# Kernel optimization log

Measured on AMD Instinct MI355X. Metric: run time of the kernel, lower is better.

The kernel has to match this reference:

```python
import jax, jax.numpy as jnp
import numpy as np

K = 20
EPS = 1e-5  # BatchNorm eps, eval mode with running_mean=0, running_var=1


def _bn(x, g, b):
    # eval-mode BatchNorm with running stats (mean=0, var=1): affine only
    return x * (g / jnp.sqrt(1.0 + EPS)) + b


def _lrelu(x):
    return jax.nn.leaky_relu(x, 0.2)


def setup_inputs() -> dict:
    key = jax.random.key(0)
    ks = jax.random.split(key, 8)
    B, N, EMB, OUT = 8, 4096, 1024, 128
    def w(k, shape):
        fan_in = shape[0]
        return (jax.random.normal(k, shape, jnp.float32) / np.sqrt(fan_in)).astype(jnp.float32)
    inp = {
        "x":  jax.random.normal(ks[0], (B, N, 3), jnp.float32),
        "W1": w(ks[1], (6, 64)),   "g1": jnp.ones(64),  "b1": jnp.zeros(64),
        "W2": w(ks[2], (64, 64)),  "g2": jnp.ones(64),  "b2": jnp.zeros(64),
        "W3": w(ks[3], (64, 128)), "g3": jnp.ones(128), "b3": jnp.zeros(128),
        "W4": w(ks[4], (128, 256)),"g4": jnp.ones(256), "b4": jnp.zeros(256),
        "W5": w(ks[5], (512, EMB)),"g5": jnp.ones(EMB), "b5": jnp.zeros(EMB),
        "L1": w(ks[6], (2 * EMB, 512)), "g6": jnp.ones(512), "b6": jnp.zeros(512),
        "L2": w(ks[7], (512, 256)), "L2b": jnp.zeros(256), "g7": jnp.ones(256), "b7": jnp.zeros(256),
        "L3": w(jax.random.fold_in(key, 99), (256, OUT)), "L3b": jnp.zeros(OUT),
    }
    return inp


def _knn_idx(pts):
    # pts: [B, 3, N]; returns indices of K nearest neighbors [B, N, K]
    inner = -2.0 * jnp.einsum('bdn,bdm->bnm', pts, pts)  # [B,N,N]
    xx = jnp.sum(pts * pts, axis=1)                       # [B,N]
    pd = -xx[:, :, None] - inner - xx[:, None, :]          # negative squared distance
    return jax.lax.top_k(pd, K)[1]                         # [B,N,K]


def reference(x, W1, g1, b1, W2, g2, b2, W3, g3, b3, W4, g4, b4,
              W5, g5, b5, L1, g6, b6, L2, L2b, g7, b7, L3, L3b):
    B, N, _ = x.shape
    pts = jnp.transpose(x, (0, 2, 1))           # [B,3,N]
    idx = _knn_idx(pts)                          # [B,N,K]

    # gather neighbor coordinates: [B,N,K,3]
    feature = jax.vmap(lambda xb, ib: xb[ib])(x, idx)
    center = jnp.broadcast_to(x[:, :, None, :], (B, N, K, 3))
    h = jnp.concatenate([feature, center], axis=-1)  # [B,N,K,6]

    h = _lrelu(_bn(jnp.einsum('bnkc,co->bnko', h, W1), g1, b1))
    x1 = jnp.max(h, axis=2)                          # [B,N,64]
    h = _lrelu(_bn(jnp.einsum('bnkc,co->bnko', h, W2), g2, b2))
    x2 = jnp.max(h, axis=2)                          # [B,N,64]
    h = _lrelu(_bn(jnp.einsum('bnkc,co->bnko', h, W3), g3, b3))
    x3 = jnp.max(h, axis=2)                          # [B,N,128]
    h = _lrelu(_bn(jnp.einsum('bnkc,co->bnko', h, W4), g4, b4))
    x4 = jnp.max(h, axis=2)                          # [B,N,256]

    hc = jnp.concatenate([x1, x2, x3, x4], axis=-1)  # [B,N,512]
    h5 = _lrelu(_bn(jnp.einsum('bnc,co->bno', hc, W5), g5, b5))  # [B,N,EMB]

    gmax = jnp.max(h5, axis=1)                       # [B,EMB]
    gavg = jnp.mean(h5, axis=1)                      # [B,EMB]
    g = jnp.concatenate([gmax, gavg], axis=-1)       # [B,2*EMB]

    f = _lrelu(_bn(g @ L1, g6, b6))                  # dropout = identity (eval)
    f = _lrelu(_bn(f @ L2 + L2b, g7, b7))
    return f @ L3 + L3b                              # [B,OUT]
```

## Files before the change

### kernel.cpp

```cpp
#include <hip/hip_runtime.h>
#include <hip/hip_bf16.h>
#include <hip/hip_fp16.h>

#define NPTS 4096
#define KNB  20
#define EPSB 1e-5f

typedef _Float16 half8  __attribute__((ext_vector_type(8)));
typedef _Float16 half2v __attribute__((ext_vector_type(2)));
typedef float    f32x4  __attribute__((ext_vector_type(4)));

__device__ __forceinline__ f32x4 mfma16(half8 a, half8 b, f32x4 c){
  return __builtin_amdgcn_mfma_f32_16x16x32_f16(a, b, c, 0, 0, 0);
}

__device__ __forceinline__ half8 loadA_lds(const _Float16* buf, int C, int mt, int ks, int lane){
  int row = mt*16 + (lane & 15);
  int k0  = ks*32 + (lane >> 4)*8;
  int e   = (row*C + k0) ^ ((row & 7) << 3);
  return *reinterpret_cast<const half8*>(&buf[e]);
}

__device__ __forceinline__ half8 loadB_g(const _Float16* WT, int K, int nt, int ks, int lane){
  int col = nt*16 + (lane & 15);
  int k0  = ks*32 + (lane >> 4)*8;
  return *reinterpret_cast<const half8*>(&WT[col*K + k0]);
}

__device__ __forceinline__ half2v pkmax(half2v a, half2v b){
  return __builtin_elementwise_max(a, b);
}
__device__ __forceinline__ half2v shflx_h2(half2v v, int m){
  int iv = __builtin_bit_cast(int, v);
  iv = __shfl_xor(iv, m);
  return __builtin_bit_cast(half2v, iv);
}
__device__ __forceinline__ half2v ep_pk(float a, float b, half2v sc2, half2v bs2){
  half2v v = __builtin_bit_cast(half2v, __builtin_amdgcn_cvt_pkrtz(a, b));
  v = v*sc2 + bs2;
  half2v w = v * (half2v){(_Float16)0.2f, (_Float16)0.2f};
  return pkmax(v, w);
}

__global__ __launch_bounds__(1024)
void knn_kernel(const float* __restrict__ x, int* __restrict__ idx_out){
  __shared__ float4 spts[NPTS];
  int b  = blockIdx.x >> 8;
  int r0 = (blockIdx.x & 255) << 4;
  const float* xb = x + (size_t)b*NPTS*3;
  for (int t = threadIdx.x; t < NPTS; t += 1024){
    float px = xb[t*3+0], py = xb[t*3+1], pz = xb[t*3+2];
    spts[t] = make_float4(px, py, pz, 0.5f*(px*px + py*py + pz*pz));
  }
  __syncthreads();
  int wave = threadIdx.x >> 6, lane = threadIdx.x & 63;
  int i = r0 + wave;
  float4 pi = spts[i];
  float b1 = -INFINITY, b2 = -INFINITY, b3 = -INFINITY;
  int   i1 = 0, i2 = 0, i3 = 0;
  #pragma unroll 8
  for (int t = 0; t < 64; ++t){
    int j = (t << 6) + lane;
    float4 q = spts[j];
    float d = pi.x*q.x + pi.y*q.y + pi.z*q.z - pi.w - q.w;
    bool c1 = d > b1, c2 = d > b2, c3 = d > b3;
    float t2 = fmaxf(b2, fminf(b1, d));
    float t3 = fmaxf(b3, fminf(b2, d));
    i3 = c2 ? i2 : (c3 ? j : i3);
    i2 = c1 ? i1 : (c2 ? j : i2);
    i1 = c1 ? j : i1;
    b1 = fmaxf(b1, d);
    b2 = t2; b3 = t3;
  }
  unsigned long long rem = 0ull;
  size_t obase = ((size_t)b*NPTS + i)*KNB;
  #pragma unroll 1
  for (int kk = 0; kk < KNB; ++kk){
    unsigned s = __float_as_uint(b1);
    unsigned key = s ^ ((unsigned)(((int)s) >> 31) | 0x80000000u);
    key = (key & 0xFFFFFFC0u) | (unsigned)lane;
    unsigned bv = key;
    #pragma unroll
    for (int m = 1; m <= 32; m <<= 1){
      unsigned ov = (unsigned)__shfl_xor((int)bv, m);
      bv = bv > ov ? bv : ov;
    }
    int wl = (int)(bv & 63u);
    int bj = __shfl(i1, wl);
    if (lane == 0) idx_out[obase + kk] = bj;
    bool iw = (lane == wl);
    unsigned long long nbit = 1ull << (i1 >> 6);
    rem |= iw ? nbit : 0ull;
    b1 = iw ? b2 : b1;  i1 = iw ? i2 : i1;
    b2 = iw ? b3 : b2;  i2 = iw ? i3 : i2;
    b3 = iw ? -INFINITY : b3;
    if (kk < KNB-1 && __any(b1 == -INFINITY)){
      if (b1 == -INFINITY){
        b2 = -INFINITY; b3 = -INFINITY; i1 = 0; i2 = 0; i3 = 0;
        #pragma unroll 8
        for (int t = 0; t < 64; ++t){
          if (rem & (1ull << t)) continue;
          int j = (t << 6) + lane;
          float4 q = spts[j];
          float d = pi.x*q.x + pi.y*q.y + pi.z*q.z - pi.w - q.w;
          bool c1 = d > b1, c2 = d > b2, c3 = d > b3;
          float t2 = fmaxf(b2, fminf(b1, d));
          float t3 = fmaxf(b3, fminf(b2, d));
          i3 = c2 ? i2 : (c3 ? j : i3);
          i2 = c1 ? i1 : (c2 ? j : i2);
          i1 = c1 ? j : i1;
          b1 = fmaxf(b1, d);
          b2 = t2; b3 = t3;
        }
      }
    }
  }
}

__global__ __launch_bounds__(256)
void prep_kernel(const float* __restrict__ W2, const float* __restrict__ W3,
                 const float* __restrict__ W4,
                 _Float16* __restrict__ W2T, _Float16* __restrict__ W3T,
                 _Float16* __restrict__ W4T){
  int t = blockIdx.x*256 + threadIdx.x;
  if (t < 4096){ int o=t>>6, k=t&63;                W2T[t] = (_Float16)W2[k*64+o]; }
  else if (t < 12288){ int u=t-4096;  int o=u>>6, k=u&63;   W3T[u] = (_Float16)W3[k*128+o]; }
  else if (t < 45056){ int u=t-12288; int o=u>>7, k=u&127;  W4T[u] = (_Float16)W4[k*256+o]; }
}

__global__ __launch_bounds__(256)
void prep5_kernel(const float* __restrict__ W5, _Float16* __restrict__ W5T){
  __shared__ float tile[32][33];
  int tk = (blockIdx.x & 15) << 5;
  int to = (blockIdx.x >> 4) << 5;
  int lr = threadIdx.x >> 5;
  int lc = threadIdx.x & 31;
  #pragma unroll
  for (int r = 0; r < 32; r += 8)
    tile[lr + r][lc] = W5[(size_t)(tk + lr + r)*1024 + to + lc];
  __syncthreads();
  #pragma unroll
  for (int r = 0; r < 32; r += 8)
    W5T[(size_t)(to + lr + r)*512 + tk + lc] = (_Float16)tile[lc][lr + r];
}

__device__ __forceinline__ void pk_bucket(int mt, bool c1, bool c2, bool c3, half2v m,
                                          half2v& q0, half2v& q1, half2v& q2, half2v& q3){
  const half2v NI = {(_Float16)-INFINITY, (_Float16)-INFINITY};
  if (mt == 0)      q0 = pkmax(q0, m);
  else if (mt == 4) q3 = pkmax(q3, m);
  else if (mt == 1){ q1 = pkmax(q1, c1 ? m : NI); q0 = pkmax(q0, c1 ? NI : m); }
  else if (mt == 2){ q2 = pkmax(q2, c2 ? m : NI); q1 = pkmax(q1, c2 ? NI : m); }
  else             { q3 = pkmax(q3, c3 ? m : NI); q2 = pkmax(q2, c3 ? NI : m); }
}

__device__ __forceinline__ void reduce_write_pk(half2v q0, half2v q1, half2v q2, half2v q3,
                                                _Float16* __restrict__ hc, size_t gp0,
                                                int off, int g, int c){
  q0 = pkmax(q0, shflx_h2(q0,16)); q0 = pkmax(q0, shflx_h2(q0,32));
  q1 = pkmax(q1, shflx_h2(q1,16)); q1 = pkmax(q1, shflx_h2(q1,32));
  q2 = pkmax(q2, shflx_h2(q2,16)); q2 = pkmax(q2, shflx_h2(q2,32));
  q3 = pkmax(q3, shflx_h2(q3,16)); q3 = pkmax(q3, shflx_h2(q3,32));
  half2v v = (g == 0) ? q0 : (g == 1) ? q1 : (g == 2) ? q2 : q3;
  _Float16 r = v.x > v.y ? v.x : v.y;
  hc[(gp0 + g)*512 + off + c] = r;
}

__global__ __launch_bounds__(256)
void edge_kernel(const float* __restrict__ x, const int* __restrict__ knn,
                 const float* __restrict__ W1, const float* __restrict__ g1, const float* __restrict__ b1,
                 const _Float16* __restrict__ W2T, const float* __restrict__ g2, const float* __restrict__ b2,
                 const _Float16* __restrict__ W3T, const float* __restrict__ g3, const float* __restrict__ b3,
                 const _Float16* __restrict__ W4T, const float* __restrict__ g4, const float* __restrict__ b4,
                 _Float16* __restrict__ hc){
  __shared__ __align__(16) char smem[40960];
  _Float16* hb1 = (_Float16*)(smem);
  _Float16* hb2 = (_Float16*)(smem + 10240);
  _Float16* hb3 = (_Float16*)(smem + 20480);
  float*    h0f = (float*)(smem + 20480);
  float*    h0c = (float*)(smem + 20480 + 1280);
  const float rs = 1.f / sqrtf(1.f + EPSB);
  const half2v NI = {(_Float16)-INFINITY, (_Float16)-INFINITY};
  int gp0 = blockIdx.x << 2;
  int b   = gp0 >> 12;
  int n0  = gp0 & (NPTS-1);
  const float* xb = x + (size_t)b*NPTS*3;
  int tid = threadIdx.x;
  if (tid < 80){
    int p = tid / 20, k = tid % 20;
    int nb = knn[((size_t)b*NPTS + n0 + p)*KNB + k];
    h0f[tid*4+0] = xb[nb*3+0];
    h0f[tid*4+1] = xb[nb*3+1];
    h0f[tid*4+2] = xb[nb*3+2];
  } else if (tid < 96){
    int u = tid - 80; int p = u >> 2, c = u & 3;
    if (c < 3) h0c[p*4+c] = xb[(n0+p)*3+c];
  }
  __syncthreads();
  int w = tid >> 6, lane = tid & 63, g = lane >> 4, cc = lane & 15;
  bool c1 = (g >= 1), c2 = (g >= 2), c3 = (g >= 3);
  {
    int col = lane;
    float sc = g1[col]*rs, bs = b1[col];
    float w0=W1[col], w1_=W1[64+col], w2_=W1[128+col], w3_=W1[192+col], w4_=W1[256+col], w5_=W1[320+col];
    float cx = h0c[w*4+0], cy = h0c[w*4+1], cz = h0c[w*4+2];
    float m1 = -INFINITY;
    #pragma unroll 5
    for (int k = 0; k < KNB; ++k){
      int r = w*20 + k;
      float a = h0f[r*4+0]*w0 + h0f[r*4+1]*w1_ + h0f[r*4+2]*w2_ + cx*w3_ + cy*w4_ + cz*w5_;
      float vv = a*sc + bs; vv = vv > 0.f ? vv : 0.2f*vv;
      hb1[((r<<6)+col) ^ ((r&7)<<3)] = (_Float16)vv;
      m1 = fmaxf(m1, vv);
    }
    hc[(size_t)(gp0 + w)*512 + col] = (_Float16)m1;
  }
  __syncthreads();
  {
    int colg = (w<<4) + cc;
    float scf = g2[colg]*rs, bsf = b2[colg];
    half2v sc2 = {(_Float16)scf,(_Float16)scf}, bs2 = {(_Float16)bsf,(_Float16)bsf};
    half8 bf0 = loadB_g(W2T, 64, w, 0, lane);
    half8 bf1 = loadB_g(W2T, 64, w, 1, lane);
    half2v q0=NI, q1=NI, q2=NI, q3=NI;
    #pragma unroll
    for (int mt = 0; mt < 5; ++mt){
      f32x4 a = {0.f,0.f,0.f,0.f};
      a = mfma16(loadA_lds(hb1,64,mt,0,lane), bf0, a);
      a = mfma16(loadA_lds(hb1,64,mt,1,lane), bf1, a);
      half2v lo = ep_pk(a[0], a[1], sc2, bs2);
      half2v hi = ep_pk(a[2], a[3], sc2, bs2);
      int r0_ = mt*16 + g*4;
      hb2[((r0_+0)*64+colg) ^ (((r0_+0)&7)<<3)] = lo.x;
      hb2[((r0_+1)*64+colg) ^ (((r0_+1)&7)<<3)] = lo.y;
      hb2[((r0_+2)*64+colg) ^ (((r0_+2)&7)<<3)] = hi.x;
      hb2[((r0_+3)*64+colg) ^ (((r0_+3)&7)<<3)] = hi.y;
      pk_bucket(mt, c1, c2, c3, pkmax(lo,hi), q0, q1, q2, q3);
    }
    reduce_write_pk(q0,q1,q2,q3, hc, gp0, 64 + (w<<4), g, cc);
  }
  __syncthreads();
  {
    int ntA = (w<<1), ntB = ntA + 1;
    int colA = (ntA<<4) + cc, colB = (ntB<<4) + cc;
    float sAf = g3[colA]*rs, bAf = b3[colA];
    float sBf = g3[colB]*rs, bBf = b3[colB];
    half2v scA2={(_Float16)sAf,(_Float16)sAf}, bsA2={(_Float16)bAf,(_Float16)bAf};
    half2v scB2={(_Float16)sBf,(_Float16)sBf}, bsB2={(_Float16)bBf,(_Float16)bBf};
    half8 bA0 = loadB_g(W3T, 64, ntA, 0, lane);
    half8 bA1 = loadB_g(W3T, 64, ntA, 1, lane);
    half8 bB0 = loadB_g(W3T, 64, ntB, 0, lane);
    half8 bB1 = loadB_g(W3T, 64, ntB, 1, lane);
    half2v qA0=NI,qA1=NI,qA2=NI,qA3=NI, qB0=NI,qB1=NI,qB2=NI,qB3=NI;
    #pragma unroll
    for (int mt = 0; mt < 5; ++mt){
      half8 a0 = loadA_lds(hb2,64,mt,0,lane);
      half8 a1 = loadA_lds(hb2,64,mt,1,lane);
      f32x4 aA = {0.f,0.f,0.f,0.f};
      aA = mfma16(a0, bA0, aA); aA = mfma16(a1, bA1, aA);
      f32x4 aB = {0.f,0.f,0.f,0.f};
      aB = mfma16(a0, bB0, aB); aB = mfma16(a1, bB1, aB);
      half2v loA = ep_pk(aA[0],aA[1],scA2,bsA2);
      half2v hiA = ep_pk(aA[2],aA[3],scA2,bsA2);
      half2v loB = ep_pk(aB[0],aB[1],scB2,bsB2);
      half2v hiB = ep_pk(aB[2],aB[3],scB2,bsB2);
      int r0_ = mt*16 + g*4;
      hb3[((r0_+0)*128+colA) ^ (((r0_+0)&7)<<3)] = loA.x;
      hb3[((r0_+1)*128+colA) ^ (((r0_+1)&7)<<3)] = loA.y;
      hb3[((r0_+2)*128+colA) ^ (((r0_+2)&7)<<3)] = hiA.x;
      hb3[((r0_+3)*128+colA) ^ (((r0_+3)&7)<<3)] = hiA.y;
      hb3[((r0_+0)*128+colB) ^ (((r0_+0)&7)<<3)] = loB.x;
      hb3[((r0_+1)*128+colB) ^ (((r0_+1)&7)<<3)] = loB.y;
      hb3[((r0_+2)*128+colB) ^ (((r0_+2)&7)<<3)] = hiB.x;
      hb3[((r0_+3)*128+colB) ^ (((r0_+3)&7)<<3)] = hiB.y;
      pk_bucket(mt, c1, c2, c3, pkmax(loA,hiA), qA0,qA1,qA2,qA3);
      pk_bucket(mt, c1, c2, c3, pkmax(loB,hiB), qB0,qB1,qB2,qB3);
    }
    reduce_write_pk(qA0,qA1,qA2,qA3, hc, gp0, 128 + (ntA<<4), g, cc);
    reduce_write_pk(qB0,qB1,qB2,qB3, hc, gp0, 128 + (ntB<<4), g, cc);
  }
  __syncthreads();
  #pragma unroll 1
  for (int pass = 0; pass < 2; ++pass){
    int ntA = (pass<<3) + w, ntB = ntA + 4;
    int colA = (ntA<<4) + cc, colB = (ntB<<4) + cc;
    float sAf = g4[colA]*rs, bAf = b4[colA];
    float sBf = g4[colB]*rs, bBf = b4[colB];
    half2v scA2={(_Float16)sAf,(_Float16)sAf}, bsA2={(_Float16)bAf,(_Float16)bAf};
    half2v scB2={(_Float16)sBf,(_Float16)sBf}, bsB2={(_Float16)bBf,(_Float16)bBf};
    half8 bwA[4], bwB[4];
    #pragma unroll
    for (int ks = 0; ks < 4; ++ks){
      bwA[ks] = loadB_g(W4T, 128, ntA, ks, lane);
      bwB[ks] = loadB_g(W4T, 128, ntB, ks, lane);
    }
    half2v qA0=NI,qA1=NI,qA2=NI,qA3=NI, qB0=NI,qB1=NI,qB2=NI,qB3=NI;
    #pragma unroll
    for (int mt = 0; mt < 5; ++mt){
      half8 a[4];
      #pragma unroll
      for (int ks = 0; ks < 4; ++ks) a[ks] = loadA_lds(hb3,128,mt,ks,lane);
      f32x4 aA = {0.f,0.f,0.f,0.f};
      #pragma unroll
      for (int ks = 0; ks < 4; ++ks) aA = mfma16(a[ks], bwA[ks], aA);
      f32x4 aB = {0.f,0.f,0.f,0.f};
      #pragma unroll
      for (int ks = 0; ks < 4; ++ks) aB = mfma16(a[ks], bwB[ks], aB);
      half2v mA = pkmax(ep_pk(aA[0],aA[1],scA2,bsA2), ep_pk(aA[2],aA[3],scA2,bsA2));
      half2v mB = pkmax(ep_pk(aB[0],aB[1],scB2,bsB2), ep_pk(aB[2],aB[3],scB2,bsB2));
      pk_bucket(mt, c1, c2, c3, mA, qA0,qA1,qA2,qA3);
      pk_bucket(mt, c1, c2, c3, mB, qB0,qB1,qB2,qB3);
    }
    reduce_write_pk(qA0,qA1,qA2,qA3, hc, gp0, 256 + (ntA<<4), g, cc);
    reduce_write_pk(qB0,qB1,qB2,qB3, hc, gp0, 256 + (ntB<<4), g, cc);
  }
}

__global__ __launch_bounds__(256)
void gemm5_kernel(const _Float16* __restrict__ hc, const _Float16* __restrict__ W5T,
                  const float* __restrict__ g5, const float* __restrict__ b5,
                  float* __restrict__ red){
  __shared__ __align__(16) _Float16 sA[64*512];
  int rowblk = blockIdx.x >> 2;
  int colblk = blockIdx.x & 3;
  int row0 = rowblk << 6;
  #pragma unroll 1
  for (int it = 0; it < 16; ++it){
    int eoff = it*2048 + threadIdx.x*8;
    int row = eoff >> 9;
    int ine = eoff & 511;
    half8 vsrc = *reinterpret_cast<const half8*>(
        &hc[(size_t)(row0 + row)*512 + (ine ^ ((row & 7) << 3))]);
    *reinterpret_cast<half8*>(&sA[(row << 9) + ine]) = vsrc;
  }
  __syncthreads();
  int wave = threadIdx.x >> 6, lane = threadIdx.x & 63;
  f32x4 acc[4][4] = {};
  #pragma unroll 1
  for (int ks = 0; ks < 16; ++ks){
    half8 af[4];
    #pragma unroll
    for (int mt = 0; mt < 4; ++mt) af[mt] = loadA_lds(sA, 512, mt, ks, lane);
    #pragma unroll
    for (int nt = 0; nt < 4; ++nt){
      int ntg = (colblk<<4) + (wave<<2) + nt;
      half8 bf = loadB_g(W5T, 512, ntg, ks, lane);
      #pragma unroll
      for (int mt = 0; mt < 4; ++mt)
        acc[mt][nt] = mfma16(af[mt], bf, acc[mt][nt]);
    }
  }
  int batch = row0 >> 12;
  int chunk = (row0 & (NPTS-1)) >> 6;
  const float rs = 1.f/sqrtf(1.f+EPSB);
  #pragma unroll
  for (int nt = 0; nt < 4; ++nt){
    int ntg = (colblk<<4) + (wave<<2) + nt;
    int colg = (ntg<<4) + (lane & 15);
    float sc = g5[colg]*rs, bs = b5[colg];
    float vmax = -INFINITY, vsum = 0.f;
    #pragma unroll
    for (int mt = 0; mt < 4; ++mt){
      #pragma unroll
      for (int r = 0; r < 4; ++r){
        float vv = acc[mt][nt][r]*sc + bs;
        vv = vv>0.f ? vv : 0.2f*vv;
        vmax = fmaxf(vmax, vv); vsum += vv;
      }
    }
    vmax = fmaxf(vmax, __shfl_xor(vmax, 16)); vsum += __shfl_xor(vsum, 16);
    vmax = fmaxf(vmax, __shfl_xor(vmax, 32)); vsum += __shfl_xor(vsum, 32);
    if ((lane >> 4) == 0){
      size_t base = (size_t)((batch<<6) + chunk)*2048;
      red[base + colg] = vmax;
      red[base + 1024 + colg] = vsum;
    }
  }
}

__global__ __launch_bounds__(256)
void reduce_g_kernel(const float* __restrict__ red, float* __restrict__ g){
  int t = blockIdx.x*256 + threadIdx.x;
  int b = t >> 10, col = t & 1023;
  float m = -INFINITY, s = 0.f;
  #pragma unroll 4
  for (int c = 0; c < 64; ++c){
    size_t base = (size_t)((b<<6)+c)*2048;
    m = fmaxf(m, red[base + col]);
    s += red[base + 1024 + col];
  }
  g[(b<<11) + col]        = m;
  g[(b<<11) + 1024 + col] = s * (1.f/4096.f);
}

__global__ __launch_bounds__(256)
void fc1_kernel(const float* __restrict__ g, const float* __restrict__ L1,
                const float* __restrict__ g6, const float* __restrict__ b6,
                float* __restrict__ f1){
  __shared__ float part[4][64];
  int b  = blockIdx.x >> 3;
  int og = blockIdx.x & 7;
  int o  = (og << 6) + (threadIdx.x & 63);
  int kg = threadIdx.x >> 6;
  const float* gb = g + (b << 11);
  float acc = 0.f;
  #pragma unroll 8
  for (int k = kg*512; k < kg*512 + 512; ++k) acc += gb[k]*L1[k*512 + o];
  part[kg][threadIdx.x & 63] = acc;
  __syncthreads();
  if (threadIdx.x < 64){
    float s = part[0][threadIdx.x] + part[1][threadIdx.x] + part[2][threadIdx.x] + part[3][threadIdx.x];
    float v = s*(g6[o]/sqrtf(1.f+EPSB)) + b6[o];
    f1[(b<<9) + o] = v > 0.f ? v : 0.2f*v;
  }
}

__global__ __launch_bounds__(256)
void fc2_kernel(const float* __restrict__ f1, const float* __restrict__ L2, const float* __restrict__ L2b,
                const float* __restrict__ g7, const float* __restrict__ b7, float* __restrict__ f2){
  __shared__ float part[4][64];
  int b  = blockIdx.x >> 2;
  int og = blockIdx.x & 3;
  int o  = (og << 6) + (threadIdx.x & 63);
  int kg = threadIdx.x >> 6;
  const float* fb = f1 + (b << 9);
  float acc = 0.f;
  #pragma unroll 8
  for (int k = kg*128; k < kg*128 + 128; ++k) acc += fb[k]*L2[k*256 + o];
  part[kg][threadIdx.x & 63] = acc;
  __syncthreads();
  if (threadIdx.x < 64){
    float s = part[0][threadIdx.x] + part[1][threadIdx.x] + part[2][threadIdx.x] + part[3][threadIdx.x];
    float v = (s + L2b[o])*(g7[o]/sqrtf(1.f+EPSB)) + b7[o];
    f2[(b<<8) + o] = v > 0.f ? v : 0.2f*v;
  }
}

__global__ __launch_bounds__(256)
void fc3_kernel(const float* __restrict__ f2, const float* __restrict__ L3, const float* __restrict__ L3b,
                float* __restrict__ out){
  __shared__ float part[2][128];
  int b  = blockIdx.x;
  int o  = threadIdx.x & 127;
  int kg = threadIdx.x >> 7;
  const float* fb = f2 + (b << 8);
  float acc = 0.f;
  #pragma unroll 8
  for (int k = kg*128; k < kg*128 + 128; ++k) acc += fb[k]*L3[k*128 + o];
  part[kg][o] = acc;
  __syncthreads();
  if (threadIdx.x < 128)
    out[(b<<7) + o] = part[0][o] + part[1][o] + L3b[o];
}

extern "C" void kernel_launch(void* const* d_in, const int* in_sizes, int n_in,
                              void* d_out, int out_size, void* d_ws, size_t ws_size,
                              hipStream_t stream){
  const float* x  = (const float*)d_in[0];
  const float* W1 = (const float*)d_in[1];
  const float* g1 = (const float*)d_in[2];  const float* b1 = (const float*)d_in[3];
  const float* W2 = (const float*)d_in[4];
  const float* g2 = (const float*)d_in[5];  const float* b2 = (const float*)d_in[6];
  const float* W3 = (const float*)d_in[7];
  const float* g3 = (const float*)d_in[8];  const float* b3 = (const float*)d_in[9];
  const float* W4 = (const float*)d_in[10];
  const float* g4 = (const float*)d_in[11]; const float* b4 = (const float*)d_in[12];
  const float* W5 = (const float*)d_in[13];
  const float* g5 = (const float*)d_in[14]; const float* b5 = (const float*)d_in[15];
  const float* L1 = (const float*)d_in[16];
  const float* g6 = (const float*)d_in[17]; const float* b6 = (const float*)d_in[18];
  const float* L2 = (const float*)d_in[19]; const float* L2b = (const float*)d_in[20];
  const float* g7 = (const float*)d_in[21]; const float* b7 = (const float*)d_in[22];
  const float* L3 = (const float*)d_in[23]; const float* L3b = (const float*)d_in[24];

  char* ws = (char*)d_ws;
  int*      idx  = (int*)(ws + 0);
  _Float16* hc   = (_Float16*)(ws + 2621440);
  _Float16* W2T  = (_Float16*)(ws + 36175872);
  _Float16* W3T  = (_Float16*)(ws + 36184064);
  _Float16* W4T  = (_Float16*)(ws + 36200448);
  _Float16* W5T  = (_Float16*)(ws + 36265984);
  float*    red  = (float*)(ws + 37314560);
  float*    gbuf = (float*)(ws + 41508864);
  float*    f1   = (float*)(ws + 41574400);
  float*    f2   = (float*)(ws + 41590784);

  knn_kernel<<<2048, 1024, 0, stream>>>(x, idx);
  prep_kernel<<<176, 256, 0, stream>>>(W2, W3, W4, W2T, W3T, W4T);
  prep5_kernel<<<512, 256, 0, stream>>>(W5, W5T);
  edge_kernel<<<8192, 256, 0, stream>>>(x, idx, W1, g1, b1, W2T, g2, b2,
                                        W3T, g3, b3, W4T, g4, b4, hc);
  gemm5_kernel<<<2048, 256, 0, stream>>>(hc, W5T, g5, b5, red);
  reduce_g_kernel<<<32, 256, 0, stream>>>(red, gbuf);
  fc1_kernel<<<64, 256, 0, stream>>>(gbuf, L1, g6, b6, f1);
  fc2_kernel<<<32, 256, 0, stream>>>(f1, L2, L2b, g7, b7, f2);
  fc3_kernel<<<8, 256, 0, stream>>>(f2, L3, L3b, (float*)d_out);
}
```

Baseline: 426.5 us.

## Fuse KNN search into edge-conv kernel, reading precomputed float4 points from global

Removes the standalone KNN kernel and does the neighbor search inside the edge-conv kernel: each wave finds the top-20 neighbours for its point and writes the indices to shared memory, so the index buffer no longer goes through global memory. A small pre-kernel packs the points into float4 with half squared norm, and the fused kernel streams those candidates from global memory (served by L2/L1) rather than staging them in LDS. The cost is that the edge kernel's occupancy and latency now include the KNN scan, and candidate loads hit the cache instead of LDS.

```diff
diff --git a/kernel.cpp b/kernel.cpp
--- a/kernel.cpp
+++ b/kernel.cpp
@@ -42,79 +42,11 @@
   return pkmax(v, w);
 }
 
-__global__ __launch_bounds__(1024)
-void knn_kernel(const float* __restrict__ x, int* __restrict__ idx_out){
-  __shared__ float4 spts[NPTS];
-  int b  = blockIdx.x >> 8;
-  int r0 = (blockIdx.x & 255) << 4;
-  const float* xb = x + (size_t)b*NPTS*3;
-  for (int t = threadIdx.x; t < NPTS; t += 1024){
-    float px = xb[t*3+0], py = xb[t*3+1], pz = xb[t*3+2];
-    spts[t] = make_float4(px, py, pz, 0.5f*(px*px + py*py + pz*pz));
-  }
-  __syncthreads();
-  int wave = threadIdx.x >> 6, lane = threadIdx.x & 63;
-  int i = r0 + wave;
-  float4 pi = spts[i];
-  float b1 = -INFINITY, b2 = -INFINITY, b3 = -INFINITY;
-  int   i1 = 0, i2 = 0, i3 = 0;
-  #pragma unroll 8
-  for (int t = 0; t < 64; ++t){
-    int j = (t << 6) + lane;
-    float4 q = spts[j];
-    float d = pi.x*q.x + pi.y*q.y + pi.z*q.z - pi.w - q.w;
-    bool c1 = d > b1, c2 = d > b2, c3 = d > b3;
-    float t2 = fmaxf(b2, fminf(b1, d));
-    float t3 = fmaxf(b3, fminf(b2, d));
-    i3 = c2 ? i2 : (c3 ? j : i3);
-    i2 = c1 ? i1 : (c2 ? j : i2);
-    i1 = c1 ? j : i1;
-    b1 = fmaxf(b1, d);
-    b2 = t2; b3 = t3;
-  }
-  unsigned long long rem = 0ull;
-  size_t obase = ((size_t)b*NPTS + i)*KNB;
-  #pragma unroll 1
-  for (int kk = 0; kk < KNB; ++kk){
-    unsigned s = __float_as_uint(b1);
-    unsigned key = s ^ ((unsigned)(((int)s) >> 31) | 0x80000000u);
-    key = (key & 0xFFFFFFC0u) | (unsigned)lane;
-    unsigned bv = key;
-    #pragma unroll
-    for (int m = 1; m <= 32; m <<= 1){
-      unsigned ov = (unsigned)__shfl_xor((int)bv, m);
-      bv = bv > ov ? bv : ov;
-    }
-    int wl = (int)(bv & 63u);
-    int bj = __shfl(i1, wl);
-    if (lane == 0) idx_out[obase + kk] = bj;
-    bool iw = (lane == wl);
-    unsigned long long nbit = 1ull << (i1 >> 6);
-    rem |= iw ? nbit : 0ull;
-    b1 = iw ? b2 : b1;  i1 = iw ? i2 : i1;
-    b2 = iw ? b3 : b2;  i2 = iw ? i3 : i2;
-    b3 = iw ? -INFINITY : b3;
-    if (kk < KNB-1 && __any(b1 == -INFINITY)){
-      if (b1 == -INFINITY){
-        b2 = -INFINITY; b3 = -INFINITY; i1 = 0; i2 = 0; i3 = 0;
-        #pragma unroll 8
-        for (int t = 0; t < 64; ++t){
-          if (rem & (1ull << t)) continue;
-          int j = (t << 6) + lane;
-          float4 q = spts[j];
-          float d = pi.x*q.x + pi.y*q.y + pi.z*q.z - pi.w - q.w;
-          bool c1 = d > b1, c2 = d > b2, c3 = d > b3;
-          float t2 = fmaxf(b2, fminf(b1, d));
-          float t3 = fmaxf(b3, fminf(b2, d));
-          i3 = c2 ? i2 : (c3 ? j : i3);
-          i2 = c1 ? i1 : (c2 ? j : i2);
-          i1 = c1 ? j : i1;
-          b1 = fmaxf(b1, d);
-          b2 = t2; b3 = t3;
-        }
-      }
-    }
-  }
+__global__ __launch_bounds__(256)
+void pts4_kernel(const float* __restrict__ x, float4* __restrict__ pts4){
+  int t = blockIdx.x*256 + threadIdx.x;
+  float px = x[t*3+0], py = x[t*3+1], pz = x[t*3+2];
+  pts4[t] = make_float4(px, py, pz, 0.5f*(px*px + py*py + pz*pz));
 }
 
 __global__ __launch_bounds__(256)
@@ -167,7 +99,7 @@
 }
 
 __global__ __launch_bounds__(256)
-void edge_kernel(const float* __restrict__ x, const int* __restrict__ knn,
+void edgeknn_kernel(const float4* __restrict__ pts4,
                  const float* __restrict__ W1, const float* __restrict__ g1, const float* __restrict__ b1,
                  const _Float16* __restrict__ W2T, const float* __restrict__ g2, const float* __restrict__ b2,
                  const _Float16* __restrict__ W3T, const float* __restrict__ g3, const float* __restrict__ b3,
@@ -179,25 +111,93 @@
   _Float16* hb3 = (_Float16*)(smem + 20480);
   float*    h0f = (float*)(smem + 20480);
   float*    h0c = (float*)(smem + 20480 + 1280);
+  int*      nbidx = (int*)(smem);
   const float rs = 1.f / sqrtf(1.f + EPSB);
   const half2v NI = {(_Float16)-INFINITY, (_Float16)-INFINITY};
   int gp0 = blockIdx.x << 2;
   int b   = gp0 >> 12;
   int n0  = gp0 & (NPTS-1);
-  const float* xb = x + (size_t)b*NPTS*3;
+  const float4* pb = pts4 + ((size_t)b << 12);
   int tid = threadIdx.x;
+  int w = tid >> 6, lane = tid & 63, g = lane >> 4, cc = lane & 15;
+  {
+    int i = n0 + w;
+    float4 pi = pb[i];
+    float b1_ = -INFINITY, b2_ = -INFINITY, b3_ = -INFINITY;
+    int   i1 = 0, i2 = 0, i3 = 0;
+    #pragma unroll 8
+    for (int t = 0; t < 64; ++t){
+      int j = (t << 6) + lane;
+      float4 q = pb[j];
+      float d = pi.x*q.x + pi.y*q.y + pi.z*q.z - pi.w - q.w;
+      bool c1 = d > b1_, c2 = d > b2_, c3 = d > b3_;
+      float t2 = fmaxf(b2_, fminf(b1_, d));
+      float t3 = fmaxf(b3_, fminf(b2_, d));
+      i3 = c2 ? i2 : (c3 ? j : i3);
+      i2 = c1 ? i1 : (c2 ? j : i2);
+      i1 = c1 ? j : i1;
+      b1_ = fmaxf(b1_, d);
+      b2_ = t2; b3_ = t3;
+    }
+    unsigned long long rem = 0ull;
+    #pragma unroll 1
+    for (int kk = 0; kk < KNB; ++kk){
+      unsigned s = __float_as_uint(b1_);
+      unsigned key = s ^ ((unsigned)(((int)s) >> 31) | 0x80000000u);
+      key = (key & 0xFFFFFFC0u) | (unsigned)lane;
+      unsigned bv = key;
+      #pragma unroll
+      for (int m = 1; m <= 32; m <<= 1){
+        unsigned ov = (unsigned)__shfl_xor((int)bv, m);
+        bv = bv > ov ? bv : ov;
+      }
+      int wl = (int)(bv & 63u);
+      int bj = __shfl(i1, wl);
+      if (lane == 0) nbidx[w*KNB + kk] = bj;
+      bool iw = (lane == wl);
+      unsigned long long nbit = 1ull << (i1 >> 6);
+      rem |= iw ? nbit : 0ull;
+      b1_ = iw ? b2_ : b1_;  i1 = iw ? i2 : i1;
+      b2_ = iw ? b3_ : b2_;  i2 = iw ? i3 : i2;
+      b3_ = iw ? -INFINITY : b3_;
+      if (kk < KNB-1 && __any(b1_ == -INFINITY)){
+        if (b1_ == -INFINITY){
+          b2_ = -INFINITY; b3_ = -INFINITY; i1 = 0; i2 = 0; i3 = 0;
+          #pragma unroll 8
+          for (int t = 0; t < 64; ++t){
+            if (rem & (1ull << t)) continue;
+            int j = (t << 6) + lane;
+            float4 q = pb[j];
+            float d = pi.x*q.x + pi.y*q.y + pi.z*q.z - pi.w - q.w;
+            bool c1 = d > b1_, c2 = d > b2_, c3 = d > b3_;
+            float t2 = fmaxf(b2_, fminf(b1_, d));
+            float t3 = fmaxf(b3_, fminf(b2_, d));
+            i3 = c2 ? i2 : (c3 ? j : i3);
+            i2 = c1 ? i1 : (c2 ? j : i2);
+            i1 = c1 ? j : i1;
+            b1_ = fmaxf(b1_, d);
+            b2_ = t2; b3_ = t3;
+          }
+        }
+      }
+    }
+  }
+  __syncthreads();
   if (tid < 80){
     int p = tid / 20, k = tid % 20;
-    int nb = knn[((size_t)b*NPTS + n0 + p)*KNB + k];
-    h0f[tid*4+0] = xb[nb*3+0];
-    h0f[tid*4+1] = xb[nb*3+1];
-    h0f[tid*4+2] = xb[nb*3+2];
+    int nb = nbidx[p*KNB + k];
+    float4 q = pb[nb];
+    h0f[tid*4+0] = q.x;
+    h0f[tid*4+1] = q.y;
+    h0f[tid*4+2] = q.z;
   } else if (tid < 96){
     int u = tid - 80; int p = u >> 2, c = u & 3;
-    if (c < 3) h0c[p*4+c] = xb[(n0+p)*3+c];
-  }
-  __syncthreads();
-  int w = tid >> 6, lane = tid & 63, g = lane >> 4, cc = lane & 15;
+    if (c == 0){
+      float4 q = pb[n0 + p];
+      h0c[p*4+0] = q.x; h0c[p*4+1] = q.y; h0c[p*4+2] = q.z;
+    }
+  }
+  __syncthreads();
   bool c1 = (g >= 1), c2 = (g >= 2), c3 = (g >= 3);
   {
     int col = lane;
@@ -474,7 +474,7 @@
   const float* L3 = (const float*)d_in[23]; const float* L3b = (const float*)d_in[24];
 
   char* ws = (char*)d_ws;
-  int*      idx  = (int*)(ws + 0);
+  float4*   pts4 = (float4*)(ws + 0);
   _Float16* hc   = (_Float16*)(ws + 2621440);
   _Float16* W2T  = (_Float16*)(ws + 36175872);
   _Float16* W3T  = (_Float16*)(ws + 36184064);
@@ -485,11 +485,11 @@
   float*    f1   = (float*)(ws + 41574400);
   float*    f2   = (float*)(ws + 41590784);
 
-  knn_kernel<<<2048, 1024, 0, stream>>>(x, idx);
+  pts4_kernel<<<128, 256, 0, stream>>>(x, pts4);
   prep_kernel<<<176, 256, 0, stream>>>(W2, W3, W4, W2T, W3T, W4T);
   prep5_kernel<<<512, 256, 0, stream>>>(W5, W5T);
-  edge_kernel<<<8192, 256, 0, stream>>>(x, idx, W1, g1, b1, W2T, g2, b2,
-                                        W3T, g3, b3, W4T, g4, b4, hc);
+  edgeknn_kernel<<<8192, 256, 0, stream>>>(pts4, W1, g1, b1, W2T, g2, b2,
+                                           W3T, g3, b3, W4T, g4, b4, hc);
   gemm5_kernel<<<2048, 256, 0, stream>>>(hc, W5T, g5, b5, red);
   reduce_g_kernel<<<32, 256, 0, stream>>>(red, gbuf);
   fc1_kernel<<<64, 256, 0, stream>>>(gbuf, L1, g6, b6, f1);
```

Result: slower. 510.0 us (+19.6%).
